# Kernel tuning notes

Measured on AMD Instinct MI355X. Metric: run time of the kernel, lower is better.

The kernel has to match this reference:

```python
import jax, jax.numpy as jnp
import numpy as np

N = 1024      # n_nodes
S = 32        # state_dim
M = 32        # message_dim
STEPS = 5     # n_steps


def setup_inputs() -> dict:
    key = jax.random.key(0)
    ks = jax.random.split(key, 12)
    w = lambda k, shape: jax.random.normal(k, shape, jnp.float32) * 0.02
    return {
        "J": jax.random.normal(ks[0], (N, N), jnp.float32),
        "b": jax.random.normal(ks[1], (N,), jnp.float32),
        # message_passing MLP (Linear(2S+3->M), Linear(M->M), Linear(M->M))
        "W1": w(ks[2], (M, 2 * S + 3)), "b1": jnp.zeros((M,), jnp.float32),
        "W2": w(ks[3], (M, M)),         "b2": jnp.zeros((M,), jnp.float32),
        "W3": w(ks[4], (M, M)),         "b3": jnp.zeros((M,), jnp.float32),
        # GRU(input=S+M, hidden=S). h0 is always zero in the original forward,
        # so weight_hh never contributes (only bias_hh does) and is omitted.
        "W_ih": w(ks[5], (3 * S, S + M)),
        "b_ih": w(ks[6], (3 * S,)),
        "b_hh": w(ks[7], (3 * S,)),
        # readout MLP (Linear(S->M), Linear(M->M), Linear(M->2))
        "R1": w(ks[8], (M, S)),  "rb1": jnp.zeros((M,), jnp.float32),
        "R2": w(ks[9], (M, M)),  "rb2": jnp.zeros((M,), jnp.float32),
        "R3": w(ks[10], (2, M)), "rb3": jnp.zeros((2,), jnp.float32),
    }


def reference(J, b, W1, b1, W2, b2, W3, b3, W_ih, b_ih, b_hh, R1, rb1, R2, rb2, R3, rb3):
    # Split first linear over the concat [h_i, h_j, J_ij, b_i, b_j] so the
    # [N, N, 2S+3] concat tensor is never materialized.
    W1a, W1b = W1[:, :S], W1[:, S:2 * S]
    wJ, wbi, wbj = W1[:, 2 * S], W1[:, 2 * S + 1], W1[:, 2 * S + 2]

    def step(h, _):
        hi = h @ W1a.T                       # [N, M] (sender part)
        hj = h @ W1b.T                       # [N, M] (receiver part)
        pre = (hi[:, None, :] + hj[None, :, :]
               + J[:, :, None] * wJ
               + b[:, None, None] * wbi
               + b[None, :, None] * wbj
               + b1)                          # [N, N, M]
        x = jax.nn.relu(pre)
        x = jax.nn.relu(x @ W2.T + b2)
        x = jax.nn.relu(x @ W3.T + b3)       # message_i_j: [N, N, M]
        m = x.sum(0)                          # message to node j: sum over senders i
        # GRU with zero initial hidden state: h' = (1-z) * n_gate
        gi = jnp.concatenate([h, m], axis=-1) @ W_ih.T + b_ih  # [N, 3S]
        r = jax.nn.sigmoid(gi[:, :S] + b_hh[:S])
        z = jax.nn.sigmoid(gi[:, S:2 * S] + b_hh[S:2 * S])
        n = jnp.tanh(gi[:, 2 * S:] + r * b_hh[2 * S:])
        return (1.0 - z) * n, None

    h0 = jnp.zeros((N, S), J.dtype)
    h, _ = jax.lax.scan(step, h0, None, length=STEPS)

    r = jax.nn.relu(h @ R1.T + rb1)
    r = jax.nn.relu(r @ R2.T + rb2)
    r = jax.nn.relu(r @ R3.T + rb3)          # [N, 2]
    return jax.nn.sigmoid(r)
```

## Files before the change

### kernel.cpp

```cpp
#include <hip/hip_runtime.h>
#include <math.h>

#define NN 1024

typedef __attribute__((ext_vector_type(8))) short bf16x8;
typedef __attribute__((ext_vector_type(4))) short bf16x4;
typedef __attribute__((ext_vector_type(4))) float f32x4;
typedef __attribute__((ext_vector_type(2))) float f32x2;
typedef __attribute__((ext_vector_type(4))) unsigned int u32x4;

#if __has_builtin(__builtin_amdgcn_mfma_f32_16x16x16bf16_1k)
#define HAVE_MFMA16 1
#define MFMA16(a, b, c) __builtin_amdgcn_mfma_f32_16x16x16bf16_1k((a), (b), (c), 0, 0, 0)
#else
#define HAVE_MFMA16 0
#endif

__device__ __forceinline__ float sigmoidf_(float x) { return 1.0f / (1.0f + __expf(-x)); }

__device__ __forceinline__ unsigned int pk2(float a, float b) {
    return __builtin_amdgcn_perm(__float_as_uint(a) + 0x8000u,
                                 __float_as_uint(b) + 0x8000u, 0x03020706u);
}
__device__ __forceinline__ unsigned int pkcvt(float a, float b) {
#if __has_builtin(__builtin_amdgcn_cvt_pk_bf16_f32)
    return __builtin_bit_cast(unsigned int, __builtin_amdgcn_cvt_pk_bf16_f32(a, b));
#else
    return pk2(a, b);
#endif
}
__device__ __forceinline__ unsigned short f2bf_rne(float a) {
    unsigned int ua = __float_as_uint(a);
    ua += 0x7fffu + ((ua >> 16) & 1u);
    return (unsigned short)(ua >> 16);
}
__device__ __forceinline__ unsigned int pk2b(float a, float b) {
    return (unsigned int)f2bf_rne(a) | ((unsigned int)f2bf_rne(b) << 16);
}

template<int S0>
__global__ __launch_bounds__(256, 4) void k_step(
    const float* __restrict__ J, const float* __restrict__ b,
    const float* __restrict__ W1, const float* __restrict__ b1,
    const float* __restrict__ W2, const float* __restrict__ b2,
    const float* __restrict__ W3, const float* __restrict__ b3,
    const float* __restrict__ Wih, const float* __restrict__ bih,
    const float* __restrict__ bhh,
    const float* __restrict__ R1, const float* __restrict__ rb1,
    const float* __restrict__ R2, const float* __restrict__ rb2,
    const float* __restrict__ R3, const float* __restrict__ rb3,
    float* __restrict__ h, float* __restrict__ v,
    const float* __restrict__ ui, float* __restrict__ uo,
    float* __restrict__ out, int do_out)
{
    __shared__ float jcol[1024];
    __shared__ float bcol[1024];
    __shared__ float red[128];
    __shared__ float hm[64], gbuf[96], hnb[32], tb[32];

    const int tid = threadIdx.x;
    const int w = tid >> 6;
    const int l = tid & 63;
    const int p = l & 15;
    const int q = l >> 4;
    const int j = blockIdx.x;

#pragma unroll
    for (int k = 0; k < 4; k++)
        jcol[k * 256 + tid] = J[(size_t)(k * 256 + tid) * NN + j];
    if (S0) {
#pragma unroll
        for (int k = 0; k < 4; k++)
            bcol[k * 256 + tid] = b[k * 256 + tid];
    }

    union FU { bf16x8 v; u32x4 u4; unsigned int d[4]; } w2a0, w2a1;
#pragma unroll
    for (int i = 0; i < 4; i++) {
        w2a0.d[i] = pk2b(W2[p * 32 + q * 8 + 2 * i],        W2[p * 32 + q * 8 + 2 * i + 1]);
        w2a1.d[i] = pk2b(W2[(16 + p) * 32 + q * 8 + 2 * i], W2[(16 + p) * 32 + q * 8 + 2 * i + 1]);
    }
    f32x4 b2v0, b2v1;
#pragma unroll
    for (int r = 0; r < 4; r++) { b2v0[r] = b2[q * 4 + r]; b2v1[r] = b2[16 + q * 4 + r]; }
    f32x2 wj2[4], wbi2[4];
#pragma unroll
    for (int i = 0; i < 4; i++) {
        wj2[i] = f32x2{W1[(q * 8 + 2 * i) * 67 + 64], W1[(q * 8 + 2 * i + 1) * 67 + 64]};
        if (S0)
            wbi2[i] = f32x2{W1[(q * 8 + 2 * i) * 67 + 65], W1[(q * 8 + 2 * i + 1) * 67 + 65]};
    }

#if HAVE_MFMA16
    union B4 { bf16x4 v; unsigned int d[2]; } B0a, B1a, B0b, B1b;
    B0a.d[0] = pk2b(W3[p * 32 + 4 * q + 0],      W3[p * 32 + 4 * q + 1]);
    B0a.d[1] = pk2b(W3[p * 32 + 4 * q + 2],      W3[p * 32 + 4 * q + 3]);
    B1a.d[0] = pk2b(W3[p * 32 + 16 + 4 * q + 0], W3[p * 32 + 16 + 4 * q + 1]);
    B1a.d[1] = pk2b(W3[p * 32 + 16 + 4 * q + 2], W3[p * 32 + 16 + 4 * q + 3]);
    B0b.d[0] = pk2b(W3[(16 + p) * 32 + 4 * q + 0],      W3[(16 + p) * 32 + 4 * q + 1]);
    B0b.d[1] = pk2b(W3[(16 + p) * 32 + 4 * q + 2],      W3[(16 + p) * 32 + 4 * q + 3]);
    B1b.d[0] = pk2b(W3[(16 + p) * 32 + 16 + 4 * q + 0], W3[(16 + p) * 32 + 16 + 4 * q + 1]);
    B1b.d[1] = pk2b(W3[(16 + p) * 32 + 16 + 4 * q + 2], W3[(16 + p) * 32 + 16 + 4 * q + 3]);
    f32x4 b3lo, b3hi;
#pragma unroll
    for (int r = 0; r < 4; r++) { b3lo[r] = b3[p]; b3hi[r] = b3[16 + p]; }
#else
    union FU w3a0, w3a1;
#pragma unroll
    for (int i = 0; i < 4; i++) {
        w3a0.d[i] = pk2b(W3[p * 32 + q * 8 + 2 * i],        W3[p * 32 + q * 8 + 2 * i + 1]);
        w3a1.d[i] = pk2b(W3[(16 + p) * 32 + q * 8 + 2 * i], W3[(16 + p) * 32 + q * 8 + 2 * i + 1]);
    }
    f32x4 b3v0, b3v1;
#pragma unroll
    for (int r = 0; r < 4; r++) { b3v0[r] = b3[q * 4 + r]; b3v1[r] = b3[16 + q * 4 + r]; }
    const int s0 = (p | ((l & 16) << 1)) << 2;
    const int s1 = s0 + 64;
    const bool qlo = (l & 32) == 0;
#endif

    f32x2 vv2[4];
    if (S0) {
        const float bj = b[j];
#pragma unroll
        for (int i = 0; i < 4; i++) {
            int m0 = q * 8 + 2 * i;
            vv2[i] = f32x2{fmaf(bj, W1[m0 * 67 + 66], b1[m0]),
                           fmaf(bj, W1[(m0 + 1) * 67 + 66], b1[m0 + 1])};
        }
    } else {
        float4 va = *(const float4*)(v + j * 32 + q * 8);
        float4 vb = *(const float4*)(v + j * 32 + q * 8 + 4);
        vv2[0] = f32x2{va.x, va.y}; vv2[1] = f32x2{va.z, va.w};
        vv2[2] = f32x2{vb.x, vb.y}; vv2[3] = f32x2{vb.z, vb.w};
    }

    f32x4 acc0 = {0.f, 0.f, 0.f, 0.f}, acc1 = {0.f, 0.f, 0.f, 0.f};
    const int ibase = w * 256;

    auto do_half = [&](float jw, f32x2 s0v, f32x2 s1v, f32x2 s2v, f32x2 s3v) {
        const f32x2 jw2v = {jw, jw};
        const f32x2 z2 = {0.f, 0.f};
        const f32x4 z4 = {0.f, 0.f, 0.f, 0.f};
        f32x2 x0 = jw2v * wj2[0] + s0v;
        f32x2 x1 = jw2v * wj2[1] + s1v;
        f32x2 x2 = jw2v * wj2[2] + s2v;
        f32x2 x3 = jw2v * wj2[3] + s3v;
        x0 = __builtin_elementwise_max(x0, z2);
        x1 = __builtin_elementwise_max(x1, z2);
        x2 = __builtin_elementwise_max(x2, z2);
        x3 = __builtin_elementwise_max(x3, z2);

        union BU { u32x4 u4; bf16x8 v; unsigned int d[4]; } bx;
        bx.d[0] = pkcvt(x0[0], x0[1]);
        bx.d[1] = pkcvt(x1[0], x1[1]);
        bx.d[2] = pkcvt(x2[0], x2[1]);
        bx.d[3] = pkcvt(x3[0], x3[1]);

        f32x4 c0 = __builtin_amdgcn_mfma_f32_16x16x32_bf16(w2a0.v, bx.v, b2v0, 0, 0, 0);
        f32x4 c1 = __builtin_amdgcn_mfma_f32_16x16x32_bf16(w2a1.v, bx.v, b2v1, 0, 0, 0);
        c0 = __builtin_elementwise_max(c0, z4);
        c1 = __builtin_elementwise_max(c1, z4);

#if HAVE_MFMA16
        union B4 { bf16x4 v; unsigned int d[2]; } A0, A1;
        A0.d[0] = pkcvt(c0[0], c0[1]); A0.d[1] = pkcvt(c0[2], c0[3]);
        A1.d[0] = pkcvt(c1[0], c1[1]); A1.d[1] = pkcvt(c1[2], c1[3]);

        f32x4 e0 = MFMA16(A0.v, B0a.v, b3lo);
        e0 = MFMA16(A1.v, B1a.v, e0);
        f32x4 e1 = MFMA16(A0.v, B0b.v, b3hi);
        e1 = MFMA16(A1.v, B1b.v, e1);
        acc0 = acc0 + __builtin_elementwise_max(e0, z4);
        acc1 = acc1 + __builtin_elementwise_max(e1, z4);
#else
        const int d0 = (int)pkcvt(c0[0], c0[1]);
        const int d1 = (int)pkcvt(c0[2], c0[3]);
        const int d2 = (int)pkcvt(c1[0], c1[1]);
        const int d3 = (int)pkcvt(c1[2], c1[3]);
        const int A0_ = __builtin_amdgcn_ds_bpermute(s0, d0);
        const int A1_ = __builtin_amdgcn_ds_bpermute(s0, d1);
        const int A2_ = __builtin_amdgcn_ds_bpermute(s1, d0);
        const int A3_ = __builtin_amdgcn_ds_bpermute(s1, d1);
        const int B0_ = __builtin_amdgcn_ds_bpermute(s0, d2);
        const int B1_ = __builtin_amdgcn_ds_bpermute(s0, d3);
        const int B2_ = __builtin_amdgcn_ds_bpermute(s1, d2);
        const int B3_ = __builtin_amdgcn_ds_bpermute(s1, d3);
        union BU yr;
        yr.d[0] = (unsigned)(qlo ? A0_ : B0_);
        yr.d[1] = (unsigned)(qlo ? A1_ : B1_);
        yr.d[2] = (unsigned)(qlo ? A2_ : B2_);
        yr.d[3] = (unsigned)(qlo ? A3_ : B3_);
        f32x4 e0 = __builtin_amdgcn_mfma_f32_16x16x32_bf16(w3a0.v, yr.v, b3v0, 0, 0, 0);
        f32x4 e1 = __builtin_amdgcn_mfma_f32_16x16x32_bf16(w3a1.v, yr.v, b3v1, 0, 0, 0);
        acc0 = acc0 + __builtin_elementwise_max(e0, z4);
        acc1 = acc1 + __builtin_elementwise_max(e1, z4);
#endif
    };

    __syncthreads();

    if (S0) {
#pragma unroll
        for (int tt = 0; tt < 8; ++tt) {
            const int rb0 = ibase + p + 32 * tt;
            const float jwA = jcol[rb0], jwB = jcol[rb0 + 16];
            const float biA = bcol[rb0], biB = bcol[rb0 + 16];
            const f32x2 bA = {biA, biA}, bB = {biB, biB};
            do_half(jwA, bA * wbi2[0] + vv2[0], bA * wbi2[1] + vv2[1],
                         bA * wbi2[2] + vv2[2], bA * wbi2[3] + vv2[3]);
            do_half(jwB, bB * wbi2[0] + vv2[0], bB * wbi2[1] + vv2[1],
                         bB * wbi2[2] + vv2[2], bB * wbi2[3] + vv2[3]);
        }
    } else {
        const float* up = ui + (size_t)(ibase + p) * 32 + q * 8;
        float4 ua0[2], ub0[2], ua1[2], ub1[2];
#pragma unroll
        for (int s = 0; s < 2; s++) {
            ua0[s] = *(const float4*)(up + (size_t)s * 1024);
            ub0[s] = *(const float4*)(up + (size_t)s * 1024 + 4);
            ua1[s] = *(const float4*)(up + (size_t)s * 1024 + 512);
            ub1[s] = *(const float4*)(up + (size_t)s * 1024 + 516);
        }
#pragma unroll
        for (int tt = 0; tt < 8; ++tt) {
            const int rb0 = ibase + p + 32 * tt;
            const float jwA = jcol[rb0], jwB = jcol[rb0 + 16];
            const int sl = tt & 1;
            const float4 uaA = ua0[sl], ubA = ub0[sl];
            const float4 uaB = ua1[sl], ubB = ub1[sl];
            if (tt < 6) {
                const float* un = up + (size_t)(tt + 2) * 1024;
                ua0[sl] = *(const float4*)(un);
                ub0[sl] = *(const float4*)(un + 4);
                ua1[sl] = *(const float4*)(un + 512);
                ub1[sl] = *(const float4*)(un + 516);
            }
            do_half(jwA, f32x2{uaA.x, uaA.y} + vv2[0], f32x2{uaA.z, uaA.w} + vv2[1],
                         f32x2{ubA.x, ubA.y} + vv2[2], f32x2{ubA.z, ubA.w} + vv2[3]);
            do_half(jwB, f32x2{uaB.x, uaB.y} + vv2[0], f32x2{uaB.z, uaB.w} + vv2[1],
                         f32x2{ubB.x, ubB.y} + vv2[2], f32x2{ubB.z, ubB.w} + vv2[3]);
        }
    }

#if HAVE_MFMA16
    float s0r = acc0[0] + acc0[1] + acc0[2] + acc0[3];
    float s1r = acc1[0] + acc1[1] + acc1[2] + acc1[3];
    s0r += __shfl_xor(s0r, 16);  s0r += __shfl_xor(s0r, 32);
    s1r += __shfl_xor(s1r, 16);  s1r += __shfl_xor(s1r, 32);
    if (l < 16) { red[w * 32 + l] = s0r;  red[w * 32 + 16 + l] = s1r; }
#else
#pragma unroll
    for (int bit = 1; bit < 16; bit <<= 1) {
#pragma unroll
        for (int r = 0; r < 4; r++) {
            acc0[r] += __shfl_xor(acc0[r], bit);
            acc1[r] += __shfl_xor(acc1[r], bit);
        }
    }
    if (p == 0) {
#pragma unroll
        for (int r = 0; r < 4; r++) {
            red[w * 32 + q * 4 + r]      = acc0[r];
            red[w * 32 + 16 + q * 4 + r] = acc1[r];
        }
    }
#endif
    __syncthreads();

    if (tid < 64) {
        float val;
        if (tid < 32) val = S0 ? 0.f : h[j * 32 + tid];
        else {
            int ss = tid - 32;
            val = red[ss] + red[32 + ss] + red[64 + ss] + red[96 + ss];
        }
        hm[tid] = val;
    }
    __syncthreads();

    if (tid < 192) {
        const int row = tid >> 1, half = tid & 1;
        const float* wr = Wih + row * 64 + half * 32;
        const float* hh = hm + half * 32;
        float acc = 0.f;
#pragma unroll
        for (int k4 = 0; k4 < 8; k4++) {
            float4 w4 = *(const float4*)(wr + 4 * k4);
            acc = fmaf(w4.x, hh[4 * k4 + 0], acc);
            acc = fmaf(w4.y, hh[4 * k4 + 1], acc);
            acc = fmaf(w4.z, hh[4 * k4 + 2], acc);
            acc = fmaf(w4.w, hh[4 * k4 + 3], acc);
        }
        acc += __shfl_xor(acc, 1);
        if (half == 0) gbuf[row] = acc + bih[row];
    }
    __syncthreads();

    if (tid < 32) {
        const int ss = tid;
        float r = sigmoidf_(gbuf[ss] + bhh[ss]);
        float z = sigmoidf_(gbuf[32 + ss] + bhh[32 + ss]);
        float n = tanhf(gbuf[64 + ss] + r * bhh[64 + ss]);
        float hn_ = (1.0f - z) * n;
        hnb[ss] = hn_;
        h[j * 32 + ss] = hn_;
    }
    __syncthreads();

    if (tid < 64) {
        const int ss = tid & 31;
        const bool isV = tid >= 32;
        const float bj = b[j];
        const float* wr = W1 + ss * 67 + (isV ? 32 : 0);
        float acc = isV ? fmaf(bj, W1[ss * 67 + 66], b1[ss]) : bj * W1[ss * 67 + 65];
#pragma unroll
        for (int k = 0; k < 32; k++) acc = fmaf(wr[k], hnb[k], acc);
        if (isV) v[j * 32 + ss] = acc;
        else     uo[j * 32 + ss] = acc;
    }

    if (do_out) {
        __syncthreads();
        if (tid < 32) {
            float a = rb1[tid];
            const float* rr = R1 + tid * 32;
#pragma unroll 8
            for (int k = 0; k < 32; k++) a = fmaf(rr[k], hnb[k], a);
            gbuf[tid] = fmaxf(a, 0.f);
        }
        __syncthreads();
        if (tid < 32) {
            float a = rb2[tid];
            const float* rr = R2 + tid * 32;
#pragma unroll 8
            for (int k = 0; k < 32; k++) a = fmaf(rr[k], gbuf[k], a);
            tb[tid] = fmaxf(a, 0.f);
        }
        __syncthreads();
        if (tid < 2) {
            float a = rb3[tid];
            const float* rr = R3 + tid * 32;
#pragma unroll 8
            for (int k = 0; k < 32; k++) a = fmaf(rr[k], tb[k], a);
            out[j * 2 + tid] = sigmoidf_(fmaxf(a, 0.f));
        }
    }
}

extern "C" void kernel_launch(void* const* d_in, const int* in_sizes, int n_in,
                              void* d_out, int out_size, void* d_ws, size_t ws_size,
                              hipStream_t stream)
{
    const float* J   = (const float*)d_in[0];
    const float* b   = (const float*)d_in[1];
    const float* W1  = (const float*)d_in[2];
    const float* b1  = (const float*)d_in[3];
    const float* W2  = (const float*)d_in[4];
    const float* b2  = (const float*)d_in[5];
    const float* W3  = (const float*)d_in[6];
    const float* b3  = (const float*)d_in[7];
    const float* Wih = (const float*)d_in[8];
    const float* bih = (const float*)d_in[9];
    const float* bhh = (const float*)d_in[10];
    const float* R1  = (const float*)d_in[11];
    const float* rb1 = (const float*)d_in[12];
    const float* R2  = (const float*)d_in[13];
    const float* rb2 = (const float*)d_in[14];
    const float* R3  = (const float*)d_in[15];
    const float* rb3 = (const float*)d_in[16];

    float* out = (float*)d_out;
    float* ws  = (float*)d_ws;
    float* h   = ws;
    float* v   = ws + 32768;
    float* u0  = ws + 65536;
    float* u1  = ws + 98304;

    for (int s = 0; s < 5; s++) {
        const float* ui = (s & 1) ? u1 : u0;
        float*       uo = (s & 1) ? u0 : u1;
        if (s == 0)
            k_step<1><<<1024, 256, 0, stream>>>(J, b, W1, b1, W2, b2, W3, b3,
                                                Wih, bih, bhh,
                                                R1, rb1, R2, rb2, R3, rb3,
                                                h, v, ui, uo, out, 0);
        else
            k_step<0><<<1024, 256, 0, stream>>>(J, b, W1, b1, W2, b2, W3, b3,
                                                Wih, bih, bhh,
                                                R1, rb1, R2, rb2, R3, rb3,
                                                h, v, ui, uo, out, (s == 4) ? 1 : 0);
    }
}
```

Baseline: 226.9 us.

## Fuse five step launches into one persistent kernel with hierarchical grid barrier

Replaces the five per-step kernel launches with one kernel that loops over the steps. Each block keeps its J column, b column and weights in LDS or registers across steps, and blocks synchronise through a two-level atomic grid barrier. h and the v term now stay on-chip instead of going through global memory, and u is exchanged through per-step slices read with atomic loads. The aim is to remove launch gaps and the repeated reload of the strided J column, at the cost of relying on all 1024 blocks being co-resident and of scalar atomic loads replacing float4 loads.

```diff
diff --git a/kernel.cpp b/kernel.cpp
--- a/kernel.cpp
+++ b/kernel.cpp
@@ -38,8 +38,39 @@
     return (unsigned int)f2bf_rne(a) | ((unsigned int)f2bf_rne(b) << 16);
 }
 
-template<int S0>
-__global__ __launch_bounds__(256, 4) void k_step(
+__device__ __forceinline__ void grid_barrier(unsigned* bar, unsigned phase) {
+    __syncthreads();
+    if (threadIdx.x == 0) {
+        const unsigned g = blockIdx.x >> 5;
+        unsigned* gcnt = bar + g * 16;
+        unsigned* grel = bar + 512 + g * 16;
+        unsigned* rcnt = bar + 1024;
+        unsigned* rrel = bar + 1040;
+        unsigned old = __hip_atomic_fetch_add(gcnt, 1u, __ATOMIC_RELAXED, __HIP_MEMORY_SCOPE_AGENT);
+        if (old == phase * 32u + 31u) {
+            unsigned rold = __hip_atomic_fetch_add(rcnt, 1u, __ATOMIC_RELAXED, __HIP_MEMORY_SCOPE_AGENT);
+            if (rold == phase * 32u + 31u) {
+                __hip_atomic_store(rrel, phase + 1u, __ATOMIC_RELAXED, __HIP_MEMORY_SCOPE_AGENT);
+            } else {
+                unsigned t = 0;
+                while (__hip_atomic_load(rrel, __ATOMIC_RELAXED, __HIP_MEMORY_SCOPE_AGENT) <= phase) {
+                    if (++t > (1u << 25)) break;
+                    __builtin_amdgcn_s_sleep(2);
+                }
+            }
+            __hip_atomic_store(grel, phase + 1u, __ATOMIC_RELAXED, __HIP_MEMORY_SCOPE_AGENT);
+        } else {
+            unsigned t = 0;
+            while (__hip_atomic_load(grel, __ATOMIC_RELAXED, __HIP_MEMORY_SCOPE_AGENT) <= phase) {
+                if (++t > (1u << 25)) break;
+                __builtin_amdgcn_s_sleep(2);
+            }
+        }
+    }
+    __syncthreads();
+}
+
+__global__ __launch_bounds__(256, 4) void k_all(
     const float* __restrict__ J, const float* __restrict__ b,
     const float* __restrict__ W1, const float* __restrict__ b1,
     const float* __restrict__ W2, const float* __restrict__ b2,
@@ -49,14 +80,13 @@
     const float* __restrict__ R1, const float* __restrict__ rb1,
     const float* __restrict__ R2, const float* __restrict__ rb2,
     const float* __restrict__ R3, const float* __restrict__ rb3,
-    float* __restrict__ h, float* __restrict__ v,
-    const float* __restrict__ ui, float* __restrict__ uo,
-    float* __restrict__ out, int do_out)
+    float* __restrict__ ub, unsigned* __restrict__ bar,
+    float* __restrict__ out)
 {
     __shared__ float jcol[1024];
     __shared__ float bcol[1024];
     __shared__ float red[128];
-    __shared__ float hm[64], gbuf[96], hnb[32], tb[32];
+    __shared__ float hm[64], gbuf[96], hb[32], vq[32], tb[32];
 
     const int tid = threadIdx.x;
     const int w = tid >> 6;
@@ -68,11 +98,10 @@
 #pragma unroll
     for (int k = 0; k < 4; k++)
         jcol[k * 256 + tid] = J[(size_t)(k * 256 + tid) * NN + j];
-    if (S0) {
-#pragma unroll
-        for (int k = 0; k < 4; k++)
-            bcol[k * 256 + tid] = b[k * 256 + tid];
-    }
+#pragma unroll
+    for (int k = 0; k < 4; k++)
+        bcol[k * 256 + tid] = b[k * 256 + tid];
+    if (tid < 32) hb[tid] = 0.f;
 
     union FU { bf16x8 v; u32x4 u4; unsigned int d[4]; } w2a0, w2a1;
 #pragma unroll
@@ -86,9 +115,8 @@
     f32x2 wj2[4], wbi2[4];
 #pragma unroll
     for (int i = 0; i < 4; i++) {
-        wj2[i] = f32x2{W1[(q * 8 + 2 * i) * 67 + 64], W1[(q * 8 + 2 * i + 1) * 67 + 64]};
-        if (S0)
-            wbi2[i] = f32x2{W1[(q * 8 + 2 * i) * 67 + 65], W1[(q * 8 + 2 * i + 1) * 67 + 65]};
+        wj2[i]  = f32x2{W1[(q * 8 + 2 * i) * 67 + 64], W1[(q * 8 + 2 * i + 1) * 67 + 64]};
+        wbi2[i] = f32x2{W1[(q * 8 + 2 * i) * 67 + 65], W1[(q * 8 + 2 * i + 1) * 67 + 65]};
     }
 
 #if HAVE_MFMA16
@@ -120,7 +148,7 @@
 #endif
 
     f32x2 vv2[4];
-    if (S0) {
+    {
         const float bj = b[j];
 #pragma unroll
         for (int i = 0; i < 4; i++) {
@@ -128,16 +156,12 @@
             vv2[i] = f32x2{fmaf(bj, W1[m0 * 67 + 66], b1[m0]),
                            fmaf(bj, W1[(m0 + 1) * 67 + 66], b1[m0 + 1])};
         }
-    } else {
-        float4 va = *(const float4*)(v + j * 32 + q * 8);
-        float4 vb = *(const float4*)(v + j * 32 + q * 8 + 4);
-        vv2[0] = f32x2{va.x, va.y}; vv2[1] = f32x2{va.z, va.w};
-        vv2[2] = f32x2{vb.x, vb.y}; vv2[3] = f32x2{vb.z, vb.w};
-    }
-
-    f32x4 acc0 = {0.f, 0.f, 0.f, 0.f}, acc1 = {0.f, 0.f, 0.f, 0.f};
+    }
+    __syncthreads();
+
     const int ibase = w * 256;
 
+    f32x4 acc0, acc1;
     auto do_half = [&](float jw, f32x2 s0v, f32x2 s1v, f32x2 s2v, f32x2 s3v) {
         const f32x2 jw2v = {jw, jw};
         const f32x2 z2 = {0.f, 0.f};
@@ -198,153 +222,164 @@
 #endif
     };
 
-    __syncthreads();
-
-    if (S0) {
-#pragma unroll
-        for (int tt = 0; tt < 8; ++tt) {
-            const int rb0 = ibase + p + 32 * tt;
-            const float jwA = jcol[rb0], jwB = jcol[rb0 + 16];
-            const float biA = bcol[rb0], biB = bcol[rb0 + 16];
-            const f32x2 bA = {biA, biA}, bB = {biB, biB};
-            do_half(jwA, bA * wbi2[0] + vv2[0], bA * wbi2[1] + vv2[1],
-                         bA * wbi2[2] + vv2[2], bA * wbi2[3] + vv2[3]);
-            do_half(jwB, bB * wbi2[0] + vv2[0], bB * wbi2[1] + vv2[1],
-                         bB * wbi2[2] + vv2[2], bB * wbi2[3] + vv2[3]);
-        }
-    } else {
-        const float* up = ui + (size_t)(ibase + p) * 32 + q * 8;
-        float4 ua0[2], ub0[2], ua1[2], ub1[2];
-#pragma unroll
-        for (int s = 0; s < 2; s++) {
-            ua0[s] = *(const float4*)(up + (size_t)s * 1024);
-            ub0[s] = *(const float4*)(up + (size_t)s * 1024 + 4);
-            ua1[s] = *(const float4*)(up + (size_t)s * 1024 + 512);
-            ub1[s] = *(const float4*)(up + (size_t)s * 1024 + 516);
-        }
-#pragma unroll
-        for (int tt = 0; tt < 8; ++tt) {
-            const int rb0 = ibase + p + 32 * tt;
-            const float jwA = jcol[rb0], jwB = jcol[rb0 + 16];
-            const int sl = tt & 1;
-            const float4 uaA = ua0[sl], ubA = ub0[sl];
-            const float4 uaB = ua1[sl], ubB = ub1[sl];
-            if (tt < 6) {
-                const float* un = up + (size_t)(tt + 2) * 1024;
-                ua0[sl] = *(const float4*)(un);
-                ub0[sl] = *(const float4*)(un + 4);
-                ua1[sl] = *(const float4*)(un + 512);
-                ub1[sl] = *(const float4*)(un + 516);
-            }
-            do_half(jwA, f32x2{uaA.x, uaA.y} + vv2[0], f32x2{uaA.z, uaA.w} + vv2[1],
-                         f32x2{ubA.x, ubA.y} + vv2[2], f32x2{ubA.z, ubA.w} + vv2[3]);
-            do_half(jwB, f32x2{uaB.x, uaB.y} + vv2[0], f32x2{uaB.z, uaB.w} + vv2[1],
-                         f32x2{ubB.x, ubB.y} + vv2[2], f32x2{ubB.z, ubB.w} + vv2[3]);
-        }
-    }
+    for (int sstep = 0; sstep < 5; ++sstep) {
+        acc0 = f32x4{0.f, 0.f, 0.f, 0.f};
+        acc1 = f32x4{0.f, 0.f, 0.f, 0.f};
+
+        if (sstep == 0) {
+#pragma unroll
+            for (int tt = 0; tt < 8; ++tt) {
+                const int rb0 = ibase + p + 32 * tt;
+                const float jwA = jcol[rb0], jwB = jcol[rb0 + 16];
+                const float biA = bcol[rb0], biB = bcol[rb0 + 16];
+                const f32x2 bA = {biA, biA}, bB = {biB, biB};
+                do_half(jwA, bA * wbi2[0] + vv2[0], bA * wbi2[1] + vv2[1],
+                             bA * wbi2[2] + vv2[2], bA * wbi2[3] + vv2[3]);
+                do_half(jwB, bB * wbi2[0] + vv2[0], bB * wbi2[1] + vv2[1],
+                             bB * wbi2[2] + vv2[2], bB * wbi2[3] + vv2[3]);
+            }
+        } else {
+            const float* up = ub + (size_t)(sstep - 1) * 32768
+                                 + (size_t)(ibase + p) * 32 + q * 8;
+            float uA[2][8], uB[2][8];
+#pragma unroll
+            for (int sl = 0; sl < 2; sl++) {
+                const float* pa = up + (size_t)sl * 1024;
+#pragma unroll
+                for (int e = 0; e < 8; e++) {
+                    uA[sl][e] = __hip_atomic_load(pa + e,       __ATOMIC_RELAXED, __HIP_MEMORY_SCOPE_AGENT);
+                    uB[sl][e] = __hip_atomic_load(pa + 512 + e, __ATOMIC_RELAXED, __HIP_MEMORY_SCOPE_AGENT);
+                }
+            }
+#pragma unroll
+            for (int tt = 0; tt < 8; ++tt) {
+                const int sl = tt & 1;
+                const int rb0 = ibase + p + 32 * tt;
+                const float jwA = jcol[rb0], jwB = jcol[rb0 + 16];
+                float cA[8], cB[8];
+#pragma unroll
+                for (int e = 0; e < 8; e++) { cA[e] = uA[sl][e]; cB[e] = uB[sl][e]; }
+                if (tt < 6) {
+                    const float* pn = up + (size_t)(tt + 2) * 1024;
+#pragma unroll
+                    for (int e = 0; e < 8; e++) {
+                        uA[sl][e] = __hip_atomic_load(pn + e,       __ATOMIC_RELAXED, __HIP_MEMORY_SCOPE_AGENT);
+                        uB[sl][e] = __hip_atomic_load(pn + 512 + e, __ATOMIC_RELAXED, __HIP_MEMORY_SCOPE_AGENT);
+                    }
+                }
+                do_half(jwA, f32x2{cA[0], cA[1]} + vv2[0], f32x2{cA[2], cA[3]} + vv2[1],
+                             f32x2{cA[4], cA[5]} + vv2[2], f32x2{cA[6], cA[7]} + vv2[3]);
+                do_half(jwB, f32x2{cB[0], cB[1]} + vv2[0], f32x2{cB[2], cB[3]} + vv2[1],
+                             f32x2{cB[4], cB[5]} + vv2[2], f32x2{cB[6], cB[7]} + vv2[3]);
+            }
+        }
 
 #if HAVE_MFMA16
-    float s0r = acc0[0] + acc0[1] + acc0[2] + acc0[3];
-    float s1r = acc1[0] + acc1[1] + acc1[2] + acc1[3];
-    s0r += __shfl_xor(s0r, 16);  s0r += __shfl_xor(s0r, 32);
-    s1r += __shfl_xor(s1r, 16);  s1r += __shfl_xor(s1r, 32);
-    if (l < 16) { red[w * 32 + l] = s0r;  red[w * 32 + 16 + l] = s1r; }
+        float s0r = acc0[0] + acc0[1] + acc0[2] + acc0[3];
+        float s1r = acc1[0] + acc1[1] + acc1[2] + acc1[3];
+        s0r += __shfl_xor(s0r, 16);  s0r += __shfl_xor(s0r, 32);
+        s1r += __shfl_xor(s1r, 16);  s1r += __shfl_xor(s1r, 32);
+        if (l < 16) { red[w * 32 + l] = s0r;  red[w * 32 + 16 + l] = s1r; }
 #else
 #pragma unroll
-    for (int bit = 1; bit < 16; bit <<= 1) {
-#pragma unroll
-        for (int r = 0; r < 4; r++) {
-            acc0[r] += __shfl_xor(acc0[r], bit);
-            acc1[r] += __shfl_xor(acc1[r], bit);
-        }
-    }
-    if (p == 0) {
-#pragma unroll
-        for (int r = 0; r < 4; r++) {
-            red[w * 32 + q * 4 + r]      = acc0[r];
-            red[w * 32 + 16 + q * 4 + r] = acc1[r];
-        }
-    }
+        for (int bit = 1; bit < 16; bit <<= 1) {
+#pragma unroll
+            for (int r = 0; r < 4; r++) {
+                acc0[r] += __shfl_xor(acc0[r], bit);
+                acc1[r] += __shfl_xor(acc1[r], bit);
+            }
+        }
+        if (p == 0) {
+#pragma unroll
+            for (int r = 0; r < 4; r++) {
+                red[w * 32 + q * 4 + r]      = acc0[r];
+                red[w * 32 + 16 + q * 4 + r] = acc1[r];
+            }
+        }
 #endif
-    __syncthreads();
-
-    if (tid < 64) {
-        float val;
-        if (tid < 32) val = S0 ? 0.f : h[j * 32 + tid];
-        else {
-            int ss = tid - 32;
-            val = red[ss] + red[32 + ss] + red[64 + ss] + red[96 + ss];
-        }
-        hm[tid] = val;
-    }
-    __syncthreads();
-
-    if (tid < 192) {
-        const int row = tid >> 1, half = tid & 1;
-        const float* wr = Wih + row * 64 + half * 32;
-        const float* hh = hm + half * 32;
-        float acc = 0.f;
-#pragma unroll
-        for (int k4 = 0; k4 < 8; k4++) {
-            float4 w4 = *(const float4*)(wr + 4 * k4);
-            acc = fmaf(w4.x, hh[4 * k4 + 0], acc);
-            acc = fmaf(w4.y, hh[4 * k4 + 1], acc);
-            acc = fmaf(w4.z, hh[4 * k4 + 2], acc);
-            acc = fmaf(w4.w, hh[4 * k4 + 3], acc);
-        }
-        acc += __shfl_xor(acc, 1);
-        if (half == 0) gbuf[row] = acc + bih[row];
-    }
-    __syncthreads();
-
+        __syncthreads();
+
+        if (tid < 64) {
+            float val;
+            if (tid < 32) val = hb[tid];
+            else {
+                int ss = tid - 32;
+                val = red[ss] + red[32 + ss] + red[64 + ss] + red[96 + ss];
+            }
+            hm[tid] = val;
+        }
+        __syncthreads();
+
+        if (tid < 192) {
+            const int row = tid >> 1, half = tid & 1;
+            const float* wr = Wih + row * 64 + half * 32;
+            const float* hh = hm + half * 32;
+            float acc = 0.f;
+#pragma unroll
+            for (int k4 = 0; k4 < 8; k4++) {
+                float4 w4 = *(const float4*)(wr + 4 * k4);
+                acc = fmaf(w4.x, hh[4 * k4 + 0], acc);
+                acc = fmaf(w4.y, hh[4 * k4 + 1], acc);
+                acc = fmaf(w4.z, hh[4 * k4 + 2], acc);
+                acc = fmaf(w4.w, hh[4 * k4 + 3], acc);
+            }
+            acc += __shfl_xor(acc, 1);
+            if (half == 0) gbuf[row] = acc + bih[row];
+        }
+        __syncthreads();
+
+        if (tid < 32) {
+            const int ss = tid;
+            float r = sigmoidf_(gbuf[ss] + bhh[ss]);
+            float z = sigmoidf_(gbuf[32 + ss] + bhh[32 + ss]);
+            float n = tanhf(gbuf[64 + ss] + r * bhh[64 + ss]);
+            hb[ss] = (1.0f - z) * n;
+        }
+        __syncthreads();
+
+        if (sstep < 4) {
+            if (tid < 64) {
+                const int ss = tid & 31;
+                const bool isV = tid >= 32;
+                const float bj = bcol[j];
+                const float* wr = W1 + ss * 67 + (isV ? 32 : 0);
+                float acc = isV ? fmaf(bj, W1[ss * 67 + 66], b1[ss]) : bj * W1[ss * 67 + 65];
+#pragma unroll
+                for (int k = 0; k < 32; k++) acc = fmaf(wr[k], hb[k], acc);
+                if (isV) vq[ss] = acc;
+                else __hip_atomic_store(ub + (size_t)sstep * 32768 + j * 32 + ss, acc,
+                                        __ATOMIC_RELAXED, __HIP_MEMORY_SCOPE_AGENT);
+            }
+            grid_barrier(bar, (unsigned)sstep);
+#pragma unroll
+            for (int i = 0; i < 4; i++)
+                vv2[i] = f32x2{vq[q * 8 + 2 * i], vq[q * 8 + 2 * i + 1]};
+        }
+    }
+
+    __syncthreads();
     if (tid < 32) {
-        const int ss = tid;
-        float r = sigmoidf_(gbuf[ss] + bhh[ss]);
-        float z = sigmoidf_(gbuf[32 + ss] + bhh[32 + ss]);
-        float n = tanhf(gbuf[64 + ss] + r * bhh[64 + ss]);
-        float hn_ = (1.0f - z) * n;
-        hnb[ss] = hn_;
-        h[j * 32 + ss] = hn_;
-    }
-    __syncthreads();
-
-    if (tid < 64) {
-        const int ss = tid & 31;
-        const bool isV = tid >= 32;
-        const float bj = b[j];
-        const float* wr = W1 + ss * 67 + (isV ? 32 : 0);
-        float acc = isV ? fmaf(bj, W1[ss * 67 + 66], b1[ss]) : bj * W1[ss * 67 + 65];
-#pragma unroll
-        for (int k = 0; k < 32; k++) acc = fmaf(wr[k], hnb[k], acc);
-        if (isV) v[j * 32 + ss] = acc;
-        else     uo[j * 32 + ss] = acc;
-    }
-
-    if (do_out) {
-        __syncthreads();
-        if (tid < 32) {
-            float a = rb1[tid];
-            const float* rr = R1 + tid * 32;
+        float a = rb1[tid];
+        const float* rr = R1 + tid * 32;
 #pragma unroll 8
-            for (int k = 0; k < 32; k++) a = fmaf(rr[k], hnb[k], a);
-            gbuf[tid] = fmaxf(a, 0.f);
-        }
-        __syncthreads();
-        if (tid < 32) {
-            float a = rb2[tid];
-            const float* rr = R2 + tid * 32;
+        for (int k = 0; k < 32; k++) a = fmaf(rr[k], hb[k], a);
+        gbuf[tid] = fmaxf(a, 0.f);
+    }
+    __syncthreads();
+    if (tid < 32) {
+        float a = rb2[tid];
+        const float* rr = R2 + tid * 32;
 #pragma unroll 8
-            for (int k = 0; k < 32; k++) a = fmaf(rr[k], gbuf[k], a);
-            tb[tid] = fmaxf(a, 0.f);
-        }
-        __syncthreads();
-        if (tid < 2) {
-            float a = rb3[tid];
-            const float* rr = R3 + tid * 32;
+        for (int k = 0; k < 32; k++) a = fmaf(rr[k], gbuf[k], a);
+        tb[tid] = fmaxf(a, 0.f);
+    }
+    __syncthreads();
+    if (tid < 2) {
+        float a = rb3[tid];
+        const float* rr = R3 + tid * 32;
 #pragma unroll 8
-            for (int k = 0; k < 32; k++) a = fmaf(rr[k], tb[k], a);
-            out[j * 2 + tid] = sigmoidf_(fmaxf(a, 0.f));
-        }
+        for (int k = 0; k < 32; k++) a = fmaf(rr[k], tb[k], a);
+        out[j * 2 + tid] = sigmoidf_(fmaxf(a, 0.f));
     }
 }
 
@@ -372,23 +407,12 @@
 
     float* out = (float*)d_out;
     float* ws  = (float*)d_ws;
-    float* h   = ws;
-    float* v   = ws + 32768;
-    float* u0  = ws + 65536;
-    float* u1  = ws + 98304;
-
-    for (int s = 0; s < 5; s++) {
-        const float* ui = (s & 1) ? u1 : u0;
-        float*       uo = (s & 1) ? u0 : u1;
-        if (s == 0)
-            k_step<1><<<1024, 256, 0, stream>>>(J, b, W1, b1, W2, b2, W3, b3,
-                                                Wih, bih, bhh,
-                                                R1, rb1, R2, rb2, R3, rb3,
-                                                h, v, ui, uo, out, 0);
-        else
-            k_step<0><<<1024, 256, 0, stream>>>(J, b, W1, b1, W2, b2, W3, b3,
-                                                Wih, bih, bhh,
-                                                R1, rb1, R2, rb2, R3, rb3,
-                                                h, v, ui, uo, out, (s == 4) ? 1 : 0);
-    }
-}
+    float* ubuf = ws;
+    unsigned* bar = (unsigned*)(ws + 4 * 32768);
+
+    hipMemsetAsync(bar, 0, 8192, stream);
+    k_all<<<1024, 256, 0, stream>>>(J, b, W1, b1, W2, b2, W3, b3,
+                                    Wih, bih, bhh,
+                                    R1, rb1, R2, rb2, R3, rb3,
+                                    ubuf, bar, out);
+}
```

After: 392.9 us. +73.2%, slower.
